# Performance work log

Measured on AMD Instinct MI355X. Metric: run time of the kernel, lower is better.

Reference implementation:

```python
import jax, jax.numpy as jnp
import numpy as np

NUM_HEADS = 8          # from init_kwargs
MASK_VALUE = -1e6      # torch code sets masked scores to -1e6 (not -inf)


def setup_inputs() -> dict:
    key = jax.random.key(0)
    k1, k2, k3, k4, k5 = jax.random.split(key, 5)
    n, S, d = 256, 512, 128   # n = B(2) * num_windows(16) * num_heads(8)
    W = 16                    # num_windows
    return {
        "queries": jax.random.normal(k1, (n, S, d), jnp.float32),
        "keys": jax.random.normal(k2, (n, S, d), jnp.float32),
        "values": jax.random.normal(k3, (n, S, d), jnp.float32),
        "valid_lens": jax.random.randint(k4, (n,), 0, S, jnp.int32),
        "window_mask": jax.random.normal(k5, (W, S, S), jnp.float32),
    }


def reference(queries, keys, values, valid_lens, window_mask):
    n, Q, d = queries.shape
    Wn, _, K = window_mask.shape
    # scaled QK^T: [n, Q, K]
    scores = jnp.einsum('bqd,bkd->bqk', queries, keys) / jnp.sqrt(
        jnp.asarray(d, queries.dtype))
    # additive window mask, broadcast over (batch, heads)
    B = n // (Wn * NUM_HEADS)
    scores = scores.reshape(B, Wn, NUM_HEADS, Q, K) + window_mask[None, :, None]
    scores = scores.reshape(n, Q, K)
    # valid-length masking: positions >= valid_lens[b] set to -1e6 before softmax
    mask = jnp.arange(K)[None, None, :] < valid_lens[:, None, None]  # [n,1,K]
    scores = jnp.where(mask, scores, MASK_VALUE)
    attn = jax.nn.softmax(scores, axis=-1)
    # dropout p=0.0 (eval) -> identity
    return jnp.einsum('bqk,bkd->bqd', attn, values)
```

## Files before the change

### kernel.cpp

```cpp
#include <hip/hip_runtime.h>

typedef unsigned short u16;
using bf16x8 = __attribute__((ext_vector_type(8))) short;
using f32x4  = __attribute__((ext_vector_type(4))) float;
using s16x4  = __attribute__((ext_vector_type(4))) short;

#define S_LEN 512
#define D_DIM 128
#define CB    32
#define KS    136
#define VS    36
#define KBUF  (CB * KS)
#define VBUF  (D_DIM * VS)
#define SCALE 0.08838834764831845f

__device__ __forceinline__ unsigned int cvt_pk_bf16(float lo, float hi) {
  unsigned int r;
  asm("v_cvt_pk_bf16_f32 %0, %1, %2" : "=v"(r) : "v"(lo), "v"(hi));
  return r;
}
__device__ __forceinline__ bf16x8 pack8(f32x4 a, f32x4 b) {
  union { unsigned int u[4]; bf16x8 v; } r;
  r.u[0] = cvt_pk_bf16(a[0], a[1]);
  r.u[1] = cvt_pk_bf16(a[2], a[3]);
  r.u[2] = cvt_pk_bf16(b[0], b[1]);
  r.u[3] = cvt_pk_bf16(b[2], b[3]);
  return r.v;
}

__global__ __launch_bounds__(256, 3)
void attn_fused(const float* __restrict__ Q, const float* __restrict__ K,
                const float* __restrict__ V, const int* __restrict__ VL,
                const float* __restrict__ WM, float* __restrict__ O) {
  __shared__ short smem[2 * KBUF + 2 * VBUF];

  const int bid  = blockIdx.x;
  const int n    = (bid & 7) | ((bid >> 6) << 3);
  const int qt   = (bid >> 3) & 7;
  const int tid  = threadIdx.x;
  const int wave = tid >> 6;
  const int L    = tid & 63;
  const int quad = L >> 4;
  const int lq   = L & 15;
  const int qw   = qt * 64 + wave * 16;
  const int qg   = qw + lq;
  const int w    = (n >> 3) & 15;

  short* K0 = smem;
  short* K1 = smem + KBUF;
  short* V0 = smem + 2 * KBUF;
  short* V1 = V0 + VBUF;

  const float* Qn  = Q + (size_t)n * S_LEN * D_DIM;
  const float* Kn  = K + (size_t)n * S_LEN * D_DIM;
  const float* Vn  = V + (size_t)n * S_LEN * D_DIM;
  const float* WMq = WM + ((size_t)w * S_LEN + qg) * S_LEN;

  const int vlen  = VL[n];
  const int kvlim = (vlen == 0) ? S_LEN : vlen;
  const int nch   = (kvlim + CB - 1) / CB;
  const int nchm1 = nch - 1;

  bf16x8 qf[4];
#pragma unroll
  for (int dc = 0; dc < 4; ++dc) {
    const f32x4* qp = (const f32x4*)(Qn + (size_t)qg * D_DIM + dc * 32 + quad * 8);
    qf[dc] = pack8(qp[0], qp[1]);
  }

  f32x4 o[8];
#pragma unroll
  for (int t = 0; t < 8; ++t) o[t] = (f32x4){0.f, 0.f, 0.f, 0.f};
  float mrun = -1e30f, lrun = 0.f;

  const int tr = tid >> 4;
  const int cc = tid & 15;
  const int colsw = (cc & 7) << 2;
  const float* Kst = Kn + (size_t)tr * D_DIM + cc * 8;
  const float* Vst = Vn + (size_t)tr * D_DIM + cc * 8;

  f32x4 Ak0a, Ak0b, Ak1a, Ak1b, Av0a, Av0b, Av1a, Av1b;
  f32x4 Bk0a, Bk0b, Bk1a, Bk1b, Bv0a, Bv0b, Bv1a, Bv1b;

#define STAGE_ISSUE(P, cb_) {                                           \
    const float* kp0 = Kst + (size_t)(cb_) * D_DIM;                     \
    const float* kp1 = kp0 + 16 * D_DIM;                                \
    const float* vp0 = Vst + (size_t)(cb_) * D_DIM;                     \
    const float* vp1 = vp0 + 16 * D_DIM;                                \
    P##k0a = ((const f32x4*)kp0)[0]; P##k0b = ((const f32x4*)kp0)[1];   \
    P##k1a = ((const f32x4*)kp1)[0]; P##k1b = ((const f32x4*)kp1)[1];   \
    P##v0a = ((const f32x4*)vp0)[0]; P##v0b = ((const f32x4*)vp0)[1];   \
    P##v1a = ((const f32x4*)vp1)[0]; P##v1b = ((const f32x4*)vp1)[1]; }

#define STAGE_WRITE(P, kd, vd) {                                        \
    *(bf16x8*)((kd) + tr * KS + cc * 8)        = pack8(P##k0a, P##k0b); \
    *(bf16x8*)((kd) + (16 + tr) * KS + cc * 8) = pack8(P##k1a, P##k1b); \
    short* vt0 = (vd) + (cc * 8) * VS + (tr ^ colsw);                   \
    short* vt1 = (vd) + (cc * 8) * VS + ((16 + tr) ^ colsw);            \
    unsigned int wa0 = cvt_pk_bf16(P##v0a[0], P##v0a[1]);               \
    unsigned int wa1 = cvt_pk_bf16(P##v0a[2], P##v0a[3]);               \
    unsigned int wa2 = cvt_pk_bf16(P##v0b[0], P##v0b[1]);               \
    unsigned int wa3 = cvt_pk_bf16(P##v0b[2], P##v0b[3]);               \
    vt0[0 * VS] = (short)(wa0);  vt0[1 * VS] = (short)(wa0 >> 16);      \
    vt0[2 * VS] = (short)(wa1);  vt0[3 * VS] = (short)(wa1 >> 16);      \
    vt0[4 * VS] = (short)(wa2);  vt0[5 * VS] = (short)(wa2 >> 16);      \
    vt0[6 * VS] = (short)(wa3);  vt0[7 * VS] = (short)(wa3 >> 16);      \
    unsigned int wb0 = cvt_pk_bf16(P##v1a[0], P##v1a[1]);               \
    unsigned int wb1 = cvt_pk_bf16(P##v1a[2], P##v1a[3]);               \
    unsigned int wb2 = cvt_pk_bf16(P##v1b[0], P##v1b[1]);               \
    unsigned int wb3 = cvt_pk_bf16(P##v1b[2], P##v1b[3]);               \
    vt1[0 * VS] = (short)(wb0);  vt1[1 * VS] = (short)(wb0 >> 16);      \
    vt1[2 * VS] = (short)(wb1);  vt1[3 * VS] = (short)(wb1 >> 16);      \
    vt1[4 * VS] = (short)(wb2);  vt1[5 * VS] = (short)(wb2 >> 16);      \
    vt1[6 * VS] = (short)(wb3);  vt1[7 * VS] = (short)(wb3 >> 16); }

  auto compute_chunk = [&](int cb, const short* Kc, const short* Vc) {
    f32x4 wm0 = *(const f32x4*)(WMq + cb + quad * 4);
    f32x4 wm1 = *(const f32x4*)(WMq + cb + 16 + quad * 4);

    f32x4 a0 = {0, 0, 0, 0}, a1 = {0, 0, 0, 0};
#pragma unroll
    for (int dc = 0; dc < 4; ++dc) {
      bf16x8 kf0 = *(const bf16x8*)(Kc + lq * KS + dc * 32 + quad * 8);
      bf16x8 kf1 = *(const bf16x8*)(Kc + (16 + lq) * KS + dc * 32 + quad * 8);
      a0 = __builtin_amdgcn_mfma_f32_16x16x32_bf16(kf0, qf[dc], a0, 0, 0, 0);
      a1 = __builtin_amdgcn_mfma_f32_16x16x32_bf16(kf1, qf[dc], a1, 0, 0, 0);
    }
    float s0[4], s1[4];
    float mloc = -1e30f;
#pragma unroll
    for (int r = 0; r < 4; ++r) {
      int k0i = cb + quad * 4 + r;
      s0[r] = (k0i < vlen)      ? a0[r] * SCALE + wm0[r] : -1e6f;
      s1[r] = (k0i + 16 < vlen) ? a1[r] * SCALE + wm1[r] : -1e6f;
      mloc = fmaxf(mloc, fmaxf(s0[r], s1[r]));
    }
    mloc = fmaxf(mloc, __shfl_xor(mloc, 16, 64));
    mloc = fmaxf(mloc, __shfl_xor(mloc, 32, 64));
    const float mnew  = fmaxf(mrun, mloc);
    const float alpha = __expf(mrun - mnew);
    mrun = mnew;

    float ev[8];
#pragma unroll
    for (int r = 0; r < 4; ++r) {
      ev[r]     = __expf(s0[r] - mnew);
      ev[4 + r] = __expf(s1[r] - mnew);
    }
    union { unsigned int u[4]; bf16x8 v; } pfu;
    pfu.u[0] = cvt_pk_bf16(ev[0], ev[1]);
    pfu.u[1] = cvt_pk_bf16(ev[2], ev[3]);
    pfu.u[2] = cvt_pk_bf16(ev[4], ev[5]);
    pfu.u[3] = cvt_pk_bf16(ev[6], ev[7]);
    float psum = 0.f;
#pragma unroll
    for (int t2 = 0; t2 < 4; ++t2) {
      union { unsigned int i; float f; } lo, hi;
      lo.i = pfu.u[t2] << 16;
      hi.i = pfu.u[t2] & 0xffff0000u;
      psum += lo.f + hi.f;
    }
    psum += __shfl_xor(psum, 16, 64);
    psum += __shfl_xor(psum, 32, 64);
    lrun = lrun * alpha + psum;

    float ar[4];
#pragma unroll
    for (int r = 0; r < 4; ++r) ar[r] = __shfl(alpha, quad * 4 + r, 64);

    const bf16x8 pf = pfu.v;
#pragma unroll
    for (int t = 0; t < 8; ++t) {
      int d   = 16 * t + lq;
      int swz = ((d >> 3) & 7) << 2;
      s16x4 b0 = *(const s16x4*)(Vc + d * VS + ((quad * 4) ^ swz));
      s16x4 b1 = *(const s16x4*)(Vc + d * VS + ((16 + quad * 4) ^ swz));
      bf16x8 bv = {b0[0], b0[1], b0[2], b0[3], b1[0], b1[1], b1[2], b1[3]};
      f32x4 ot = o[t];
#pragma unroll
      for (int r = 0; r < 4; ++r) ot[r] *= ar[r];
      o[t] = __builtin_amdgcn_mfma_f32_16x16x32_bf16(pf, bv, ot, 0, 0, 0);
    }
  };

  STAGE_ISSUE(A, 0);
  {
    const int c1 = (1 <= nchm1 ? 1 : nchm1) * CB;
    STAGE_ISSUE(B, c1);
  }
  STAGE_WRITE(A, K0, V0);
  asm volatile("s_waitcnt lgkmcnt(0)" ::: "memory");
  __builtin_amdgcn_s_barrier();

  int ci = 0;
  for (;;) {
    {
      const int cp = (ci + 2 <= nchm1 ? ci + 2 : nchm1) * CB;
      STAGE_ISSUE(A, cp);
      __builtin_amdgcn_sched_barrier(0);
      compute_chunk(ci * CB, K0, V0);
      if (ci + 1 >= nch) break;
      __builtin_amdgcn_sched_barrier(0);
      STAGE_WRITE(B, K1, V1);
      asm volatile("s_waitcnt lgkmcnt(0)" ::: "memory");
      __builtin_amdgcn_s_barrier();
    }
    {
      const int cp = (ci + 3 <= nchm1 ? ci + 3 : nchm1) * CB;
      STAGE_ISSUE(B, cp);
      __builtin_amdgcn_sched_barrier(0);
      compute_chunk((ci + 1) * CB, K1, V1);
      if (ci + 2 >= nch) break;
      __builtin_amdgcn_sched_barrier(0);
      STAGE_WRITE(A, K0, V0);
      asm volatile("s_waitcnt lgkmcnt(0)" ::: "memory");
      __builtin_amdgcn_s_barrier();
    }
    ci += 2;
  }

  asm volatile("s_waitcnt lgkmcnt(0)" ::: "memory");
  __builtin_amdgcn_s_barrier();

  float linv[4];
#pragma unroll
  for (int r = 0; r < 4; ++r) {
    float lr = __shfl(lrun, quad * 4 + r, 64);
    linv[r] = 1.f / lr;
  }
  float* ow = (float*)smem + wave * (16 * 132);
#pragma unroll
  for (int t = 0; t < 8; ++t) {
#pragma unroll
    for (int r = 0; r < 4; ++r) {
      ow[(quad * 4 + r) * 132 + 16 * t + lq] = o[t][r] * linv[r];
    }
  }
  asm volatile("s_waitcnt lgkmcnt(0)" ::: "memory");
  float* On = O + (size_t)n * S_LEN * D_DIM;
  const int half = L >> 5;
  const int c4   = (L & 31) * 4;
#pragma unroll
  for (int p = 0; p < 8; ++p) {
    int row = 2 * p + half;
    f32x4 v = *(const f32x4*)(ow + row * 132 + c4);
    *(f32x4*)(On + (size_t)(qw + row) * D_DIM + c4) = v;
  }
}

extern "C" void kernel_launch(void* const* d_in, const int* in_sizes, int n_in,
                              void* d_out, int out_size, void* d_ws, size_t ws_size,
                              hipStream_t stream) {
  const float* Q  = (const float*)d_in[0];
  const float* K  = (const float*)d_in[1];
  const float* V  = (const float*)d_in[2];
  const int*   VL = (const int*)d_in[3];
  const float* WM = (const float*)d_in[4];
  float* O = (float*)d_out;
  dim3 grid(256 * 8), block(256);
  attn_fused<<<grid, block, 0, stream>>>(Q, K, V, VL, WM, O);
}
```

Baseline: 247.7 us.

## Switch to persistent blocks pulling work items via atomic counter

Replaces the one-block-per-tile grid with 1024 persistent blocks that repeatedly grab (head, query-tile) items from a global atomic counter, reset by a memset before launch. Because valid_lens vary per head, per-item cost varies, and dynamic scheduling is meant to balance the load across CUs and reduce tail effects. It also raises launch_bounds occupancy to 4 blocks per CU and replaces the explicit waitcnt/sched_barrier sequences with __syncthreads. The cost is extra per-item barriers, an atomic, a memset, and a possible rise in register pressure under the new occupancy bound.

```diff
diff --git a/kernel.cpp b/kernel.cpp
--- a/kernel.cpp
+++ b/kernel.cpp
@@ -12,6 +12,7 @@
 #define VS    36
 #define KBUF  (CB * KS)
 #define VBUF  (D_DIM * VS)
+#define NITEMS 2048
 #define SCALE 0.08838834764831845f
 
 __device__ __forceinline__ unsigned int cvt_pk_bf16(float lo, float hi) {
@@ -27,60 +28,6 @@
   r.u[3] = cvt_pk_bf16(b[2], b[3]);
   return r.v;
 }
-
-__global__ __launch_bounds__(256, 3)
-void attn_fused(const float* __restrict__ Q, const float* __restrict__ K,
-                const float* __restrict__ V, const int* __restrict__ VL,
-                const float* __restrict__ WM, float* __restrict__ O) {
-  __shared__ short smem[2 * KBUF + 2 * VBUF];
-
-  const int bid  = blockIdx.x;
-  const int n    = (bid & 7) | ((bid >> 6) << 3);
-  const int qt   = (bid >> 3) & 7;
-  const int tid  = threadIdx.x;
-  const int wave = tid >> 6;
-  const int L    = tid & 63;
-  const int quad = L >> 4;
-  const int lq   = L & 15;
-  const int qw   = qt * 64 + wave * 16;
-  const int qg   = qw + lq;
-  const int w    = (n >> 3) & 15;
-
-  short* K0 = smem;
-  short* K1 = smem + KBUF;
-  short* V0 = smem + 2 * KBUF;
-  short* V1 = V0 + VBUF;
-
-  const float* Qn  = Q + (size_t)n * S_LEN * D_DIM;
-  const float* Kn  = K + (size_t)n * S_LEN * D_DIM;
-  const float* Vn  = V + (size_t)n * S_LEN * D_DIM;
-  const float* WMq = WM + ((size_t)w * S_LEN + qg) * S_LEN;
-
-  const int vlen  = VL[n];
-  const int kvlim = (vlen == 0) ? S_LEN : vlen;
-  const int nch   = (kvlim + CB - 1) / CB;
-  const int nchm1 = nch - 1;
-
-  bf16x8 qf[4];
-#pragma unroll
-  for (int dc = 0; dc < 4; ++dc) {
-    const f32x4* qp = (const f32x4*)(Qn + (size_t)qg * D_DIM + dc * 32 + quad * 8);
-    qf[dc] = pack8(qp[0], qp[1]);
-  }
-
-  f32x4 o[8];
-#pragma unroll
-  for (int t = 0; t < 8; ++t) o[t] = (f32x4){0.f, 0.f, 0.f, 0.f};
-  float mrun = -1e30f, lrun = 0.f;
-
-  const int tr = tid >> 4;
-  const int cc = tid & 15;
-  const int colsw = (cc & 7) << 2;
-  const float* Kst = Kn + (size_t)tr * D_DIM + cc * 8;
-  const float* Vst = Vn + (size_t)tr * D_DIM + cc * 8;
-
-  f32x4 Ak0a, Ak0b, Ak1a, Ak1b, Av0a, Av0b, Av1a, Av1b;
-  f32x4 Bk0a, Bk0b, Bk1a, Bk1b, Bv0a, Bv0b, Bv1a, Bv1b;
 
 #define STAGE_ISSUE(P, cb_) {                                           \
     const float* kp0 = Kst + (size_t)(cb_) * D_DIM;                     \
@@ -114,137 +61,191 @@
     vt1[4 * VS] = (short)(wb2);  vt1[5 * VS] = (short)(wb2 >> 16);      \
     vt1[6 * VS] = (short)(wb3);  vt1[7 * VS] = (short)(wb3 >> 16); }
 
-  auto compute_chunk = [&](int cb, const short* Kc, const short* Vc) {
-    f32x4 wm0 = *(const f32x4*)(WMq + cb + quad * 4);
-    f32x4 wm1 = *(const f32x4*)(WMq + cb + 16 + quad * 4);
-
-    f32x4 a0 = {0, 0, 0, 0}, a1 = {0, 0, 0, 0};
+__global__ __launch_bounds__(256, 4)
+void attn_fused(const float* __restrict__ Q, const float* __restrict__ K,
+                const float* __restrict__ V, const int* __restrict__ VL,
+                const float* __restrict__ WM, float* __restrict__ O,
+                int* __restrict__ work) {
+  __shared__ short smem[2 * KBUF + 2 * VBUF];
+  __shared__ int item_s;
+
+  const int tid  = threadIdx.x;
+  const int wave = tid >> 6;
+  const int L    = tid & 63;
+  const int quad = L >> 4;
+  const int lq   = L & 15;
+  const int tr   = tid >> 4;
+  const int cc   = tid & 15;
+  const int colsw = (cc & 7) << 2;
+
+  short* K0 = smem;
+  short* K1 = smem + KBUF;
+  short* V0 = smem + 2 * KBUF;
+  short* V1 = V0 + VBUF;
+
+  for (;;) {
+    __syncthreads();
+    if (tid == 0) item_s = atomicAdd(work, 1);
+    __syncthreads();
+    const int item = item_s;
+    if (item >= NITEMS) break;
+
+    const int n  = (item & 7) | ((item >> 6) << 3);
+    const int qt = (item >> 3) & 7;
+    const int qw = qt * 64 + wave * 16;
+    const int qg = qw + lq;
+    const int w  = (n >> 3) & 15;
+
+    const float* Qn  = Q + (size_t)n * S_LEN * D_DIM;
+    const float* Kn  = K + (size_t)n * S_LEN * D_DIM;
+    const float* Vn  = V + (size_t)n * S_LEN * D_DIM;
+    const float* WMq = WM + ((size_t)w * S_LEN + qg) * S_LEN;
+
+    const int vlen  = VL[n];
+    const int kvlim = (vlen == 0) ? S_LEN : vlen;
+    const int nch   = (kvlim + CB - 1) / CB;
+    const int nchm1 = nch - 1;
+
+    bf16x8 qf[4];
 #pragma unroll
     for (int dc = 0; dc < 4; ++dc) {
-      bf16x8 kf0 = *(const bf16x8*)(Kc + lq * KS + dc * 32 + quad * 8);
-      bf16x8 kf1 = *(const bf16x8*)(Kc + (16 + lq) * KS + dc * 32 + quad * 8);
-      a0 = __builtin_amdgcn_mfma_f32_16x16x32_bf16(kf0, qf[dc], a0, 0, 0, 0);
-      a1 = __builtin_amdgcn_mfma_f32_16x16x32_bf16(kf1, qf[dc], a1, 0, 0, 0);
-    }
-    float s0[4], s1[4];
-    float mloc = -1e30f;
+      const f32x4* qp = (const f32x4*)(Qn + (size_t)qg * D_DIM + dc * 32 + quad * 8);
+      qf[dc] = pack8(qp[0], qp[1]);
+    }
+
+    f32x4 o[8];
+#pragma unroll
+    for (int t = 0; t < 8; ++t) o[t] = (f32x4){0.f, 0.f, 0.f, 0.f};
+    float mrun = -1e30f, lrun = 0.f;
+
+    const float* Kst = Kn + (size_t)tr * D_DIM + cc * 8;
+    const float* Vst = Vn + (size_t)tr * D_DIM + cc * 8;
+
+    f32x4 Ak0a, Ak0b, Ak1a, Ak1b, Av0a, Av0b, Av1a, Av1b;
+    f32x4 Bk0a, Bk0b, Bk1a, Bk1b, Bv0a, Bv0b, Bv1a, Bv1b;
+
+    auto compute_chunk = [&](int cb, const short* Kc, const short* Vc) {
+      f32x4 wm0 = *(const f32x4*)(WMq + cb + quad * 4);
+      f32x4 wm1 = *(const f32x4*)(WMq + cb + 16 + quad * 4);
+
+      f32x4 a0 = {0, 0, 0, 0}, a1 = {0, 0, 0, 0};
+#pragma unroll
+      for (int dc = 0; dc < 4; ++dc) {
+        bf16x8 kf0 = *(const bf16x8*)(Kc + lq * KS + dc * 32 + quad * 8);
+        bf16x8 kf1 = *(const bf16x8*)(Kc + (16 + lq) * KS + dc * 32 + quad * 8);
+        a0 = __builtin_amdgcn_mfma_f32_16x16x32_bf16(kf0, qf[dc], a0, 0, 0, 0);
+        a1 = __builtin_amdgcn_mfma_f32_16x16x32_bf16(kf1, qf[dc], a1, 0, 0, 0);
+      }
+      float s0[4], s1[4];
+      float mloc = -1e30f;
+#pragma unroll
+      for (int r = 0; r < 4; ++r) {
+        int k0i = cb + quad * 4 + r;
+        s0[r] = (k0i < vlen)      ? a0[r] * SCALE + wm0[r] : -1e6f;
+        s1[r] = (k0i + 16 < vlen) ? a1[r] * SCALE + wm1[r] : -1e6f;
+        mloc = fmaxf(mloc, fmaxf(s0[r], s1[r]));
+      }
+      mloc = fmaxf(mloc, __shfl_xor(mloc, 16, 64));
+      mloc = fmaxf(mloc, __shfl_xor(mloc, 32, 64));
+      const float mnew  = fmaxf(mrun, mloc);
+      const float alpha = __expf(mrun - mnew);
+      mrun = mnew;
+
+      float ev[8];
+#pragma unroll
+      for (int r = 0; r < 4; ++r) {
+        ev[r]     = __expf(s0[r] - mnew);
+        ev[4 + r] = __expf(s1[r] - mnew);
+      }
+      union { unsigned int u[4]; bf16x8 v; } pfu;
+      pfu.u[0] = cvt_pk_bf16(ev[0], ev[1]);
+      pfu.u[1] = cvt_pk_bf16(ev[2], ev[3]);
+      pfu.u[2] = cvt_pk_bf16(ev[4], ev[5]);
+      pfu.u[3] = cvt_pk_bf16(ev[6], ev[7]);
+      float psum = 0.f;
+#pragma unroll
+      for (int t2 = 0; t2 < 4; ++t2) {
+        union { unsigned int i; float f; } lo, hi;
+        lo.i = pfu.u[t2] << 16;
+        hi.i = pfu.u[t2] & 0xffff0000u;
+        psum += lo.f + hi.f;
+      }
+      psum += __shfl_xor(psum, 16, 64);
+      psum += __shfl_xor(psum, 32, 64);
+      lrun = lrun * alpha + psum;
+
+      float ar[4];
+#pragma unroll
+      for (int r = 0; r < 4; ++r) ar[r] = __shfl(alpha, quad * 4 + r, 64);
+
+      const bf16x8 pf = pfu.v;
+#pragma unroll
+      for (int t = 0; t < 8; ++t) {
+        int d   = 16 * t + lq;
+        int swz = ((d >> 3) & 7) << 2;
+        s16x4 b0 = *(const s16x4*)(Vc + d * VS + ((quad * 4) ^ swz));
+        s16x4 b1 = *(const s16x4*)(Vc + d * VS + ((16 + quad * 4) ^ swz));
+        bf16x8 bv = {b0[0], b0[1], b0[2], b0[3], b1[0], b1[1], b1[2], b1[3]};
+        f32x4 ot = o[t];
+#pragma unroll
+        for (int r = 0; r < 4; ++r) ot[r] *= ar[r];
+        o[t] = __builtin_amdgcn_mfma_f32_16x16x32_bf16(pf, bv, ot, 0, 0, 0);
+      }
+    };
+
+    STAGE_ISSUE(A, 0);
+    {
+      const int c1 = (1 <= nchm1 ? 1 : nchm1) * CB;
+      STAGE_ISSUE(B, c1);
+    }
+    STAGE_WRITE(A, K0, V0);
+    __syncthreads();
+
+    int ci = 0;
+    for (;;) {
+      {
+        const int cp = (ci + 2 <= nchm1 ? ci + 2 : nchm1) * CB;
+        STAGE_ISSUE(A, cp);
+        compute_chunk(ci * CB, K0, V0);
+        if (ci + 1 >= nch) break;
+        STAGE_WRITE(B, K1, V1);
+        __syncthreads();
+      }
+      {
+        const int cp = (ci + 3 <= nchm1 ? ci + 3 : nchm1) * CB;
+        STAGE_ISSUE(B, cp);
+        compute_chunk((ci + 1) * CB, K1, V1);
+        if (ci + 2 >= nch) break;
+        STAGE_WRITE(A, K0, V0);
+        __syncthreads();
+      }
+      ci += 2;
+    }
+    __syncthreads();
+
+    float linv[4];
 #pragma unroll
     for (int r = 0; r < 4; ++r) {
-      int k0i = cb + quad * 4 + r;
-      s0[r] = (k0i < vlen)      ? a0[r] * SCALE + wm0[r] : -1e6f;
-      s1[r] = (k0i + 16 < vlen) ? a1[r] * SCALE + wm1[r] : -1e6f;
-      mloc = fmaxf(mloc, fmaxf(s0[r], s1[r]));
-    }
-    mloc = fmaxf(mloc, __shfl_xor(mloc, 16, 64));
-    mloc = fmaxf(mloc, __shfl_xor(mloc, 32, 64));
-    const float mnew  = fmaxf(mrun, mloc);
-    const float alpha = __expf(mrun - mnew);
-    mrun = mnew;
-
-    float ev[8];
-#pragma unroll
-    for (int r = 0; r < 4; ++r) {
-      ev[r]     = __expf(s0[r] - mnew);
-      ev[4 + r] = __expf(s1[r] - mnew);
-    }
-    union { unsigned int u[4]; bf16x8 v; } pfu;
-    pfu.u[0] = cvt_pk_bf16(ev[0], ev[1]);
-    pfu.u[1] = cvt_pk_bf16(ev[2], ev[3]);
-    pfu.u[2] = cvt_pk_bf16(ev[4], ev[5]);
-    pfu.u[3] = cvt_pk_bf16(ev[6], ev[7]);
-    float psum = 0.f;
-#pragma unroll
-    for (int t2 = 0; t2 < 4; ++t2) {
-      union { unsigned int i; float f; } lo, hi;
-      lo.i = pfu.u[t2] << 16;
-      hi.i = pfu.u[t2] & 0xffff0000u;
-      psum += lo.f + hi.f;
-    }
-    psum += __shfl_xor(psum, 16, 64);
-    psum += __shfl_xor(psum, 32, 64);
-    lrun = lrun * alpha + psum;
-
-    float ar[4];
-#pragma unroll
-    for (int r = 0; r < 4; ++r) ar[r] = __shfl(alpha, quad * 4 + r, 64);
-
-    const bf16x8 pf = pfu.v;
+      float lr = __shfl(lrun, quad * 4 + r, 64);
+      linv[r] = 1.f / lr;
+    }
+    float* ow = (float*)smem + wave * (16 * 132);
 #pragma unroll
     for (int t = 0; t < 8; ++t) {
-      int d   = 16 * t + lq;
-      int swz = ((d >> 3) & 7) << 2;
-      s16x4 b0 = *(const s16x4*)(Vc + d * VS + ((quad * 4) ^ swz));
-      s16x4 b1 = *(const s16x4*)(Vc + d * VS + ((16 + quad * 4) ^ swz));
-      bf16x8 bv = {b0[0], b0[1], b0[2], b0[3], b1[0], b1[1], b1[2], b1[3]};
-      f32x4 ot = o[t];
-#pragma unroll
-      for (int r = 0; r < 4; ++r) ot[r] *= ar[r];
-      o[t] = __builtin_amdgcn_mfma_f32_16x16x32_bf16(pf, bv, ot, 0, 0, 0);
-    }
-  };
-
-  STAGE_ISSUE(A, 0);
-  {
-    const int c1 = (1 <= nchm1 ? 1 : nchm1) * CB;
-    STAGE_ISSUE(B, c1);
-  }
-  STAGE_WRITE(A, K0, V0);
-  asm volatile("s_waitcnt lgkmcnt(0)" ::: "memory");
-  __builtin_amdgcn_s_barrier();
-
-  int ci = 0;
-  for (;;) {
-    {
-      const int cp = (ci + 2 <= nchm1 ? ci + 2 : nchm1) * CB;
-      STAGE_ISSUE(A, cp);
-      __builtin_amdgcn_sched_barrier(0);
-      compute_chunk(ci * CB, K0, V0);
-      if (ci + 1 >= nch) break;
-      __builtin_amdgcn_sched_barrier(0);
-      STAGE_WRITE(B, K1, V1);
-      asm volatile("s_waitcnt lgkmcnt(0)" ::: "memory");
-      __builtin_amdgcn_s_barrier();
-    }
-    {
-      const int cp = (ci + 3 <= nchm1 ? ci + 3 : nchm1) * CB;
-      STAGE_ISSUE(B, cp);
-      __builtin_amdgcn_sched_barrier(0);
-      compute_chunk((ci + 1) * CB, K1, V1);
-      if (ci + 2 >= nch) break;
-      __builtin_amdgcn_sched_barrier(0);
-      STAGE_WRITE(A, K0, V0);
-      asm volatile("s_waitcnt lgkmcnt(0)" ::: "memory");
-      __builtin_amdgcn_s_barrier();
-    }
-    ci += 2;
-  }
-
-  asm volatile("s_waitcnt lgkmcnt(0)" ::: "memory");
-  __builtin_amdgcn_s_barrier();
-
-  float linv[4];
-#pragma unroll
-  for (int r = 0; r < 4; ++r) {
-    float lr = __shfl(lrun, quad * 4 + r, 64);
-    linv[r] = 1.f / lr;
-  }
-  float* ow = (float*)smem + wave * (16 * 132);
-#pragma unroll
-  for (int t = 0; t < 8; ++t) {
-#pragma unroll
-    for (int r = 0; r < 4; ++r) {
-      ow[(quad * 4 + r) * 132 + 16 * t + lq] = o[t][r] * linv[r];
-    }
-  }
-  asm volatile("s_waitcnt lgkmcnt(0)" ::: "memory");
-  float* On = O + (size_t)n * S_LEN * D_DIM;
-  const int half = L >> 5;
-  const int c4   = (L & 31) * 4;
-#pragma unroll
-  for (int p = 0; p < 8; ++p) {
-    int row = 2 * p + half;
-    f32x4 v = *(const f32x4*)(ow + row * 132 + c4);
-    *(f32x4*)(On + (size_t)(qw + row) * D_DIM + c4) = v;
+#pragma unroll
+      for (int r = 0; r < 4; ++r) {
+        ow[(quad * 4 + r) * 132 + 16 * t + lq] = o[t][r] * linv[r];
+      }
+    }
+    float* On = O + (size_t)n * S_LEN * D_DIM;
+    const int half = L >> 5;
+    const int c4   = (L & 31) * 4;
+#pragma unroll
+    for (int p = 0; p < 8; ++p) {
+      int row = 2 * p + half;
+      f32x4 v = *(const f32x4*)(ow + row * 132 + c4);
+      *(f32x4*)(On + (size_t)(qw + row) * D_DIM + c4) = v;
+    }
   }
 }
 
@@ -257,6 +258,8 @@
   const int*   VL = (const int*)d_in[3];
   const float* WM = (const float*)d_in[4];
   float* O = (float*)d_out;
-  dim3 grid(256 * 8), block(256);
-  attn_fused<<<grid, block, 0, stream>>>(Q, K, V, VL, WM, O);
-}
+  int* work = (int*)d_ws;
+  hipMemsetAsync(work, 0, sizeof(int), stream);
+  dim3 grid(1024), block(256);
+  attn_fused<<<grid, block, 0, stream>>>(Q, K, V, VL, WM, O, work);
+}
```

Measured after the change: 346.8 us. 1.4x slower.
